# Kernel tuning notes

Measured on AMD Instinct MI355X. Metric: run time of the kernel, lower is better.

## Reference

```python
import jax, jax.numpy as jnp
import numpy as np

B, S, E, H = 2, 2048, 1024, 16
D = E // H  # head_dim = 64


def setup_inputs() -> dict:
    key = jax.random.key(0)
    ks = jax.random.split(key, 6)
    sc = 1.0 / np.sqrt(D)
    return {
        "x": jax.random.normal(ks[0], (B, S, E), dtype=jnp.float32),
        "Wq": jax.random.normal(ks[1], (D, D), dtype=jnp.float32) * sc,
        "Wk": jax.random.normal(ks[2], (D, D), dtype=jnp.float32) * sc,
        "Wv": jax.random.normal(ks[3], (D, D), dtype=jnp.float32) * sc,
        "Wo": jax.random.normal(ks[4], (E, E), dtype=jnp.float32) * (1.0 / np.sqrt(E)),
        "bo": jnp.zeros((E,), dtype=jnp.float32),
    }


def reference(x, Wq, Wk, Wv, Wo, bo):
    b, s, e = x.shape
    # split into heads: (B, H, S, D)
    xh = x.reshape(b, s, H, D).transpose(0, 2, 1, 3)
    # per-head linear projections (weights SHARED across heads); torch Linear: x @ W^T
    q = jnp.einsum('bhsd,ed->bhse', xh, Wq)
    k = jnp.einsum('bhsd,ed->bhse', xh, Wk)
    v = jnp.einsum('bhsd,ed->bhse', xh, Wv)
    # full attention matrix (B, H, S, S) — faithful to the naive original
    energy = jnp.einsum('bhqd,bhkd->bhqk', q, k)
    attn = jax.nn.softmax(energy / jnp.sqrt(jnp.asarray(D, x.dtype)), axis=-1)
    out = jnp.einsum('bhqk,bhkd->bhqd', attn, v)
    out = out.transpose(0, 2, 1, 3).reshape(b, s, e)
    return out @ Wo.T + bo
```

## Files before the change

kernel.cpp:

```cpp
#include <hip/hip_runtime.h>
#include <hip/hip_bf16.h>

#define B 2
#define S 2048
#define E 1024
#define H 16
#define D 64

typedef unsigned short ushort_t;
typedef __attribute__((ext_vector_type(8))) short bf16x8;
typedef __attribute__((ext_vector_type(4))) float f32x4;

static __device__ __forceinline__ ushort_t f2bf(float f) {
    union { float f; unsigned u; } v; v.f = f;
    unsigned r = v.u + 0x7fffu + ((v.u >> 16) & 1u);
    return (ushort_t)(r >> 16);
}

#define MFMA(a, b, c) __builtin_amdgcn_mfma_f32_16x16x32_bf16((a), (b), (c), 0, 0, 0)

__global__ __launch_bounds__(256) void cvt_w(
    const float* __restrict__ Wq, const float* __restrict__ Wk, const float* __restrict__ Wv,
    const float* __restrict__ Wo,
    ushort_t* __restrict__ wqb, ushort_t* __restrict__ wkb, ushort_t* __restrict__ wvb,
    ushort_t* __restrict__ wob)
{
    int gid = blockIdx.x, t = threadIdx.x;
    if (gid < 1024) {
        int i = gid * 1024 + t * 4;
        float4 f = *(const float4*)(Wo + i);
        ushort4 u; u.x = f2bf(f.x); u.y = f2bf(f.y); u.z = f2bf(f.z); u.w = f2bf(f.w);
        *(ushort4*)(wob + i) = u;
    } else {
        int idx = (gid - 1024) * 1024 + t * 4;
        int which = idx >> 12, off = idx & 4095;
        const float* src = (which == 0) ? Wq : (which == 1) ? Wk : Wv;
        ushort_t* dst    = (which == 0) ? wqb : (which == 1) ? wkb : wvb;
        float sc = (which == 0) ? 0.18033688011112042f : 1.0f;
        float4 f = *(const float4*)(src + off);
        ushort4 u; u.x = f2bf(f.x * sc); u.y = f2bf(f.y * sc);
        u.z = f2bf(f.z * sc); u.w = f2bf(f.w * sc);
        *(ushort4*)(dst + off) = u;
    }
}

__global__ __launch_bounds__(256) void qkv_proj(
    const float* __restrict__ x,
    const ushort_t* __restrict__ wq, const ushort_t* __restrict__ wk, const ushort_t* __restrict__ wv,
    ushort_t* __restrict__ q, ushort_t* __restrict__ k, ushort_t* __restrict__ vT)
{
    __shared__ ushort_t Xs[64][72];
    __shared__ ushort_t Wqs[64][72], Wks[64][72], Wvs[64][72];
    int t = threadIdx.x;
    int bh = blockIdx.y, b = bh >> 4, h = bh & 15;
    int s0 = blockIdx.x * 64;

    {
        int i = t >> 2, d0 = (t & 3) * 16;
        const float* xp = x + ((size_t)(b * S + s0 + i)) * E + h * D + d0;
        #pragma unroll
        for (int c = 0; c < 16; c += 4) {
            float4 f = *(const float4*)(xp + c);
            Xs[i][d0 + c + 0] = f2bf(f.x); Xs[i][d0 + c + 1] = f2bf(f.y);
            Xs[i][d0 + c + 2] = f2bf(f.z); Xs[i][d0 + c + 3] = f2bf(f.w);
        }
    }
    {
        int e = t >> 2, d0 = (t & 3) * 16;
        *(bf16x8*)&Wqs[e][d0]     = *(const bf16x8*)(wq + e * 64 + d0);
        *(bf16x8*)&Wqs[e][d0 + 8] = *(const bf16x8*)(wq + e * 64 + d0 + 8);
        *(bf16x8*)&Wks[e][d0]     = *(const bf16x8*)(wk + e * 64 + d0);
        *(bf16x8*)&Wks[e][d0 + 8] = *(const bf16x8*)(wk + e * 64 + d0 + 8);
        *(bf16x8*)&Wvs[e][d0]     = *(const bf16x8*)(wv + e * 64 + d0);
        *(bf16x8*)&Wvs[e][d0 + 8] = *(const bf16x8*)(wv + e * 64 + d0 + 8);
    }
    __syncthreads();

    int w = t >> 6, lane = t & 63, m = lane & 15, quad = lane >> 4;
    bf16x8 a0 = *(bf16x8*)&Xs[16 * w + m][quad * 8];
    bf16x8 a1 = *(bf16x8*)&Xs[16 * w + m][32 + quad * 8];
    f32x4 cq[4], ck[4], cv[4];
    #pragma unroll
    for (int nt = 0; nt < 4; nt++) { cq[nt] = (f32x4)0.f; ck[nt] = (f32x4)0.f; cv[nt] = (f32x4)0.f; }
    #pragma unroll
    for (int nt = 0; nt < 4; nt++) {
        bf16x8 b0, b1;
        b0 = *(bf16x8*)&Wqs[nt * 16 + m][quad * 8]; b1 = *(bf16x8*)&Wqs[nt * 16 + m][32 + quad * 8];
        cq[nt] = MFMA(a0, b0, cq[nt]); cq[nt] = MFMA(a1, b1, cq[nt]);
        b0 = *(bf16x8*)&Wks[nt * 16 + m][quad * 8]; b1 = *(bf16x8*)&Wks[nt * 16 + m][32 + quad * 8];
        ck[nt] = MFMA(a0, b0, ck[nt]); ck[nt] = MFMA(a1, b1, ck[nt]);
        b0 = *(bf16x8*)&Wvs[nt * 16 + m][quad * 8]; b1 = *(bf16x8*)&Wvs[nt * 16 + m][32 + quad * 8];
        cv[nt] = MFMA(a0, b0, cv[nt]); cv[nt] = MFMA(a1, b1, cv[nt]);
    }
    size_t base = (size_t)bh * S + s0;
    #pragma unroll
    for (int nt = 0; nt < 4; nt++)
        #pragma unroll
        for (int r = 0; r < 4; r++) {
            size_t idx = (base + 16 * w + quad * 4 + r) * D + nt * 16 + m;
            q[idx] = f2bf(cq[nt][r]);
            k[idx] = f2bf(ck[nt][r]);
        }
    __syncthreads();
    #pragma unroll
    for (int nt = 0; nt < 4; nt++)
        #pragma unroll
        for (int r = 0; r < 4; r++)
            Wvs[nt * 16 + m][16 * w + quad * 4 + r] = f2bf(cv[nt][r]);
    __syncthreads();
    {
        int d0 = t >> 2, sc = (t & 3) * 16;
        ushort_t* vp = vT + ((size_t)bh * D + d0) * S + s0 + sc;
        *(bf16x8*)(vp)     = *(bf16x8*)&Wvs[d0][sc];
        *(bf16x8*)(vp + 8) = *(bf16x8*)&Wvs[d0][sc + 8];
    }
}

__global__ __launch_bounds__(256) void flash_attn(
    const ushort_t* __restrict__ q, const ushort_t* __restrict__ k,
    const ushort_t* __restrict__ vT, ushort_t* __restrict__ ao)
{
    __shared__ ushort_t Ks[2][64][72];
    __shared__ ushort_t Vt[2][64][72];
    __shared__ ushort_t Ps[128][72];
    int t = threadIdx.x;
    int bh = blockIdx.y, b = bh >> 4, h = bh & 15;
    int q0 = blockIdx.x * 128;
    int w = t >> 6, lane = t & 63, m = lane & 15, quad = lane >> 4;

    const ushort_t* qb = q + ((size_t)bh * S + q0) * D;
    const ushort_t* kb = k + (size_t)bh * S * D;
    const ushort_t* vb = vT + (size_t)bh * D * S;

    bf16x8 qf[2][2];
    #pragma unroll
    for (int u = 0; u < 2; u++) {
        const ushort_t* qp = qb + (size_t)(w * 32 + u * 16 + m) * D;
        qf[u][0] = *(const bf16x8*)(qp + quad * 8);
        qf[u][1] = *(const bf16x8*)(qp + 32 + quad * 8);
    }

    f32x4 o_[2][4];
    float lsum[2] = {0.f, 0.f};
    #pragma unroll
    for (int u = 0; u < 2; u++)
        #pragma unroll
        for (int dt = 0; dt < 4; dt++) o_[u][dt] = (f32x4)0.f;

    int sr = t >> 2, scc = (t & 3) * 16;

    bf16x8 kp0, kp1, vp0, vp1;

    {
        const ushort_t* kp = kb + (size_t)sr * D + scc;
        const ushort_t* vp = vb + (size_t)sr * S + scc;
        kp0 = *(const bf16x8*)(kp);     kp1 = *(const bf16x8*)(kp + 8);
        vp0 = *(const bf16x8*)(vp);     vp1 = *(const bf16x8*)(vp + 8);
        *(bf16x8*)&Ks[0][sr][scc]     = kp0;
        *(bf16x8*)&Ks[0][sr][scc + 8] = kp1;
        *(bf16x8*)&Vt[0][sr][scc]     = vp0;
        *(bf16x8*)&Vt[0][sr][scc + 8] = vp1;
    }
    __syncthreads();
    {
        const ushort_t* kp = kb + (size_t)(64 + sr) * D + scc;
        const ushort_t* vp = vb + (size_t)sr * S + 64 + scc;
        kp0 = *(const bf16x8*)(kp);     kp1 = *(const bf16x8*)(kp + 8);
        vp0 = *(const bf16x8*)(vp);     vp1 = *(const bf16x8*)(vp + 8);
    }

    const int NT = S / 64;
    for (int it = 0; it < NT; it++) {
        int p = it & 1;
        if (it + 1 < NT) {
            *(bf16x8*)&Ks[1 - p][sr][scc]     = kp0;
            *(bf16x8*)&Ks[1 - p][sr][scc + 8] = kp1;
            *(bf16x8*)&Vt[1 - p][sr][scc]     = vp0;
            *(bf16x8*)&Vt[1 - p][sr][scc + 8] = vp1;
        }
        if (it + 2 < NT) {
            int k0n = (it + 2) * 64;
            const ushort_t* kp = kb + (size_t)(k0n + sr) * D + scc;
            const ushort_t* vp = vb + (size_t)sr * S + k0n + scc;
            kp0 = *(const bf16x8*)(kp);     kp1 = *(const bf16x8*)(kp + 8);
            vp0 = *(const bf16x8*)(vp);     vp1 = *(const bf16x8*)(vp + 8);
        }

        #pragma unroll
        for (int nt = 0; nt < 4; nt++) {
            bf16x8 kf0 = *(bf16x8*)&Ks[p][nt * 16 + m][quad * 8];
            bf16x8 kf1 = *(bf16x8*)&Ks[p][nt * 16 + m][32 + quad * 8];
            #pragma unroll
            for (int u = 0; u < 2; u++) {
                f32x4 c = (f32x4)0.f;
                c = MFMA(kf0, qf[u][0], c);
                c = MFMA(kf1, qf[u][1], c);
                unsigned pu[4];
                #pragma unroll
                for (int r = 0; r < 4; r++) {
                    float pv = __builtin_amdgcn_exp2f(c[r]);
                    unsigned pt = __float_as_uint(pv) & 0xffff0000u;
                    lsum[u] += __uint_as_float(pt);
                    pu[r] = pt;
                }
                unsigned pk0 = __builtin_amdgcn_perm(pu[1], pu[0], 0x07060302u);
                unsigned pk1 = __builtin_amdgcn_perm(pu[3], pu[2], 0x07060302u);
                int ql = w * 32 + u * 16 + m, cc = nt * 16 + quad * 4;
                *(uint2*)&Ps[ql][cc] = make_uint2(pk0, pk1);
            }
        }
        asm volatile("s_waitcnt lgkmcnt(0)" ::: "memory");

        bf16x8 pa[2][2];
        #pragma unroll
        for (int u = 0; u < 2; u++) {
            int ql = w * 32 + u * 16 + m;
            pa[u][0] = *(bf16x8*)&Ps[ql][quad * 8];
            pa[u][1] = *(bf16x8*)&Ps[ql][32 + quad * 8];
        }
        #pragma unroll
        for (int dt = 0; dt < 4; dt++) {
            bf16x8 vf0 = *(bf16x8*)&Vt[p][dt * 16 + m][quad * 8];
            bf16x8 vf1 = *(bf16x8*)&Vt[p][dt * 16 + m][32 + quad * 8];
            #pragma unroll
            for (int u = 0; u < 2; u++) {
                o_[u][dt] = MFMA(pa[u][0], vf0, o_[u][dt]);
                o_[u][dt] = MFMA(pa[u][1], vf1, o_[u][dt]);
            }
        }
        __syncthreads();
    }

    float inv[2][4];
    #pragma unroll
    for (int u = 0; u < 2; u++) {
        float l = lsum[u];
        l += __shfl_xor(l, 16, 64);
        l += __shfl_xor(l, 32, 64);
        #pragma unroll
        for (int r = 0; r < 4; r++)
            inv[u][r] = 1.f / __shfl(l, quad * 4 + r, 64);
    }
    #pragma unroll
    for (int u = 0; u < 2; u++)
        #pragma unroll
        for (int dt = 0; dt < 4; dt++)
            #pragma unroll
            for (int r = 0; r < 4; r++) {
                int srow = q0 + w * 32 + u * 16 + quad * 4 + r;
                ao[((size_t)(b * S + srow)) * E + h * D + dt * 16 + m] = f2bf(o_[u][dt][r] * inv[u][r]);
            }
}

__global__ __launch_bounds__(256) void out_proj(
    const ushort_t* __restrict__ A, const ushort_t* __restrict__ Wob,
    const float* __restrict__ bo, float* __restrict__ Y)
{
    __shared__ ushort_t As[128][72];
    __shared__ ushort_t Ws[64][72];
    int t = threadIdx.x;
    int n0 = blockIdx.x * 64, m0 = blockIdx.y * 128;
    int w = t >> 6, lane = t & 63, m = lane & 15, quad = lane >> 4;
    f32x4 acc[2][4];
    #pragma unroll
    for (int u = 0; u < 2; u++)
        #pragma unroll
        for (int nt = 0; nt < 4; nt++) acc[u][nt] = (f32x4)0.f;

    int ar = t >> 1, ac = (t & 1) * 32;
    int wr = t >> 2, wc = (t & 3) * 16;
    for (int k0 = 0; k0 < E; k0 += 64) {
        __syncthreads();
        {
            const ushort_t* ap = A + (size_t)(m0 + ar) * E + k0 + ac;
            #pragma unroll
            for (int i = 0; i < 4; i++)
                *(bf16x8*)&As[ar][ac + 8 * i] = *(const bf16x8*)(ap + 8 * i);
            const ushort_t* wp = Wob + (size_t)(n0 + wr) * E + k0 + wc;
            *(bf16x8*)&Ws[wr][wc]     = *(const bf16x8*)(wp);
            *(bf16x8*)&Ws[wr][wc + 8] = *(const bf16x8*)(wp + 8);
        }
        __syncthreads();
        #pragma unroll
        for (int h2 = 0; h2 < 2; h2++) {
            bf16x8 af[2];
            af[0] = *(bf16x8*)&As[w * 32 + m][h2 * 32 + quad * 8];
            af[1] = *(bf16x8*)&As[w * 32 + 16 + m][h2 * 32 + quad * 8];
            #pragma unroll
            for (int nt = 0; nt < 4; nt++) {
                bf16x8 bfr = *(bf16x8*)&Ws[nt * 16 + m][h2 * 32 + quad * 8];
                acc[0][nt] = MFMA(af[0], bfr, acc[0][nt]);
                acc[1][nt] = MFMA(af[1], bfr, acc[1][nt]);
            }
        }
    }
    #pragma unroll
    for (int u = 0; u < 2; u++)
        #pragma unroll
        for (int nt = 0; nt < 4; nt++)
            #pragma unroll
            for (int r = 0; r < 4; r++) {
                int row = m0 + w * 32 + u * 16 + quad * 4 + r;
                int col = n0 + nt * 16 + m;
                Y[(size_t)row * E + col] = acc[u][nt][r] + bo[col];
            }
}

extern "C" void kernel_launch(void* const* d_in, const int* in_sizes, int n_in,
                              void* d_out, int out_size, void* d_ws, size_t ws_size,
                              hipStream_t stream)
{
    const float* x  = (const float*)d_in[0];
    const float* Wq = (const float*)d_in[1];
    const float* Wk = (const float*)d_in[2];
    const float* Wv = (const float*)d_in[3];
    const float* Wo = (const float*)d_in[4];
    const float* bo = (const float*)d_in[5];
    float* Y = (float*)d_out;

    const size_t n = (size_t)B * H * S * D;
    ushort_t* qw  = (ushort_t*)d_ws;
    ushort_t* kw  = qw + n;
    ushort_t* vTw = kw + n;
    ushort_t* ao  = vTw + n;
    ushort_t* wob = ao + n;
    ushort_t* wqb = wob + (size_t)E * E;
    ushort_t* wkb = wqb + D * D;
    ushort_t* wvb = wkb + D * D;

    cvt_w<<<dim3(1024 + 12), 256, 0, stream>>>(Wq, Wk, Wv, Wo, wqb, wkb, wvb, wob);
    qkv_proj<<<dim3(S / 64, B * H), 256, 0, stream>>>(x, wqb, wkb, wvb, qw, kw, vTw);
    flash_attn<<<dim3(S / 128, B * H), 256, 0, stream>>>(qw, kw, vTw, ao);
    out_proj<<<dim3(E / 64, (B * S) / 128), 256, 0, stream>>>(ao, wob, bo, Y);
}
```

Before: 158.7 us.

## Use 32x32x16 MFMA in flash attention and pass P via lane shuffles

Measured after the change: 155.5 us. 1.02x faster.

```diff
diff --git a/kernel.cpp b/kernel.cpp
--- a/kernel.cpp
+++ b/kernel.cpp
@@ -10,6 +10,7 @@
 typedef unsigned short ushort_t;
 typedef __attribute__((ext_vector_type(8))) short bf16x8;
 typedef __attribute__((ext_vector_type(4))) float f32x4;
+typedef __attribute__((ext_vector_type(16))) float f32x16;
 
 static __device__ __forceinline__ ushort_t f2bf(float f) {
     union { float f; unsigned u; } v; v.f = f;
@@ -17,7 +18,9 @@
     return (ushort_t)(r >> 16);
 }
 
-#define MFMA(a, b, c) __builtin_amdgcn_mfma_f32_16x16x32_bf16((a), (b), (c), 0, 0, 0)
+#define MFMA(a, b, c)   __builtin_amdgcn_mfma_f32_16x16x32_bf16((a), (b), (c), 0, 0, 0)
+#define MFMA32(a, b, c) __builtin_amdgcn_mfma_f32_32x32x16_bf16((a), (b), (c), 0, 0, 0)
+#define PACKBF(hi, lo) __builtin_amdgcn_perm((hi), (lo), 0x07060302u)
 
 __global__ __launch_bounds__(256) void cvt_w(
     const float* __restrict__ Wq, const float* __restrict__ Wk, const float* __restrict__ Wv,
@@ -122,33 +125,26 @@
 {
     __shared__ ushort_t Ks[2][64][72];
     __shared__ ushort_t Vt[2][64][72];
-    __shared__ ushort_t Ps[128][72];
     int t = threadIdx.x;
     int bh = blockIdx.y, b = bh >> 4, h = bh & 15;
     int q0 = blockIdx.x * 128;
-    int w = t >> 6, lane = t & 63, m = lane & 15, quad = lane >> 4;
+    int w = t >> 6, lane = t & 63, l31 = lane & 31, half = lane >> 5;
 
     const ushort_t* qb = q + ((size_t)bh * S + q0) * D;
     const ushort_t* kb = k + (size_t)bh * S * D;
     const ushort_t* vb = vT + (size_t)bh * D * S;
 
-    bf16x8 qf[2][2];
-    #pragma unroll
-    for (int u = 0; u < 2; u++) {
-        const ushort_t* qp = qb + (size_t)(w * 32 + u * 16 + m) * D;
-        qf[u][0] = *(const bf16x8*)(qp + quad * 8);
-        qf[u][1] = *(const bf16x8*)(qp + 32 + quad * 8);
-    }
-
-    f32x4 o_[2][4];
-    float lsum[2] = {0.f, 0.f};
-    #pragma unroll
-    for (int u = 0; u < 2; u++)
-        #pragma unroll
-        for (int dt = 0; dt < 4; dt++) o_[u][dt] = (f32x4)0.f;
+    bf16x8 qf[4];
+    {
+        const ushort_t* qp = qb + (size_t)(w * 32 + l31) * D + half * 8;
+        #pragma unroll
+        for (int c = 0; c < 4; c++) qf[c] = *(const bf16x8*)(qp + c * 16);
+    }
+
+    f32x16 o0 = (f32x16)0.f, o1 = (f32x16)0.f;
+    float lsum = 0.f;
 
     int sr = t >> 2, scc = (t & 3) * 16;
-
     bf16x8 kp0, kp1, vp0, vp1;
 
     {
@@ -186,70 +182,61 @@
             vp0 = *(const bf16x8*)(vp);     vp1 = *(const bf16x8*)(vp + 8);
         }
 
-        #pragma unroll
-        for (int nt = 0; nt < 4; nt++) {
-            bf16x8 kf0 = *(bf16x8*)&Ks[p][nt * 16 + m][quad * 8];
-            bf16x8 kf1 = *(bf16x8*)&Ks[p][nt * 16 + m][32 + quad * 8];
-            #pragma unroll
-            for (int u = 0; u < 2; u++) {
-                f32x4 c = (f32x4)0.f;
-                c = MFMA(kf0, qf[u][0], c);
-                c = MFMA(kf1, qf[u][1], c);
-                unsigned pu[4];
-                #pragma unroll
-                for (int r = 0; r < 4; r++) {
-                    float pv = __builtin_amdgcn_exp2f(c[r]);
-                    unsigned pt = __float_as_uint(pv) & 0xffff0000u;
-                    lsum[u] += __uint_as_float(pt);
-                    pu[r] = pt;
-                }
-                unsigned pk0 = __builtin_amdgcn_perm(pu[1], pu[0], 0x07060302u);
-                unsigned pk1 = __builtin_amdgcn_perm(pu[3], pu[2], 0x07060302u);
-                int ql = w * 32 + u * 16 + m, cc = nt * 16 + quad * 4;
-                *(uint2*)&Ps[ql][cc] = make_uint2(pk0, pk1);
-            }
-        }
-        asm volatile("s_waitcnt lgkmcnt(0)" ::: "memory");
-
-        bf16x8 pa[2][2];
-        #pragma unroll
-        for (int u = 0; u < 2; u++) {
-            int ql = w * 32 + u * 16 + m;
-            pa[u][0] = *(bf16x8*)&Ps[ql][quad * 8];
-            pa[u][1] = *(bf16x8*)&Ps[ql][32 + quad * 8];
-        }
-        #pragma unroll
-        for (int dt = 0; dt < 4; dt++) {
-            bf16x8 vf0 = *(bf16x8*)&Vt[p][dt * 16 + m][quad * 8];
-            bf16x8 vf1 = *(bf16x8*)&Vt[p][dt * 16 + m][32 + quad * 8];
-            #pragma unroll
-            for (int u = 0; u < 2; u++) {
-                o_[u][dt] = MFMA(pa[u][0], vf0, o_[u][dt]);
-                o_[u][dt] = MFMA(pa[u][1], vf1, o_[u][dt]);
-            }
+        union { unsigned u[4]; bf16x8 v; } pa[4];
+        #pragma unroll
+        for (int st = 0; st < 2; st++) {
+            f32x16 e = (f32x16)0.f;
+            #pragma unroll
+            for (int c = 0; c < 4; c++) {
+                bf16x8 ka = *(bf16x8*)&Ks[p][st * 32 + l31][c * 16 + half * 8];
+                e = MFMA32(ka, qf[c], e);
+            }
+            unsigned pt[16];
+            #pragma unroll
+            for (int r = 0; r < 16; r++) {
+                float pe = __builtin_amdgcn_exp2f(e[r]);
+                unsigned msk = __float_as_uint(pe) & 0xffff0000u;
+                lsum += __uint_as_float(msk);
+                pt[r] = msk;
+            }
+            #pragma unroll
+            for (int c2 = 0; c2 < 2; c2++) {
+                int rb = c2 * 8;
+                unsigned dA = PACKBF(pt[rb + 1], pt[rb + 0]);
+                unsigned dB = PACKBF(pt[rb + 3], pt[rb + 2]);
+                unsigned dC = PACKBF(pt[rb + 5], pt[rb + 4]);
+                unsigned dD = PACKBF(pt[rb + 7], pt[rb + 6]);
+                unsigned x1 = (unsigned)__shfl_xor((int)(half ? dA : dC), 32, 64);
+                unsigned x2 = (unsigned)__shfl_xor((int)(half ? dB : dD), 32, 64);
+                int kc = st * 2 + c2;
+                pa[kc].u[0] = half ? x1 : dA;
+                pa[kc].u[1] = half ? x2 : dB;
+                pa[kc].u[2] = half ? dC : x1;
+                pa[kc].u[3] = half ? dD : x2;
+            }
+        }
+
+        #pragma unroll
+        for (int kc = 0; kc < 4; kc++) {
+            bf16x8 vf0 = *(bf16x8*)&Vt[p][l31][kc * 16 + half * 8];
+            bf16x8 vf1 = *(bf16x8*)&Vt[p][32 + l31][kc * 16 + half * 8];
+            o0 = MFMA32(pa[kc].v, vf0, o0);
+            o1 = MFMA32(pa[kc].v, vf1, o1);
         }
         __syncthreads();
     }
 
-    float inv[2][4];
-    #pragma unroll
-    for (int u = 0; u < 2; u++) {
-        float l = lsum[u];
-        l += __shfl_xor(l, 16, 64);
-        l += __shfl_xor(l, 32, 64);
-        #pragma unroll
-        for (int r = 0; r < 4; r++)
-            inv[u][r] = 1.f / __shfl(l, quad * 4 + r, 64);
-    }
-    #pragma unroll
-    for (int u = 0; u < 2; u++)
-        #pragma unroll
-        for (int dt = 0; dt < 4; dt++)
-            #pragma unroll
-            for (int r = 0; r < 4; r++) {
-                int srow = q0 + w * 32 + u * 16 + quad * 4 + r;
-                ao[((size_t)(b * S + srow)) * E + h * D + dt * 16 + m] = f2bf(o_[u][dt][r] * inv[u][r]);
-            }
+    float lfull = lsum + __shfl_xor(lsum, 32, 64);
+    float inv = 1.f / lfull;
+    #pragma unroll
+    for (int reg = 0; reg < 16; reg++) {
+        int qrow = (reg & 3) + 8 * (reg >> 2) + 4 * half;
+        float li = __shfl(inv, qrow, 64);
+        int srow = q0 + w * 32 + qrow;
+        size_t base = ((size_t)(b * S + srow)) * E + h * D + l31;
+        ao[base]      = f2bf(o0[reg] * li);
+        ao[base + 32] = f2bf(o1[reg] * li);
+    }
 }
 
 __global__ __launch_bounds__(256) void out_proj(
```
